# Optimization experiments

Measured on AMD Instinct MI355X. Metric: run time of the kernel, lower is better.

Reference implementation:

```python
import jax, jax.numpy as jnp
import numpy as np

NEG_SLOPE = 0.01  # torch nn.LeakyReLU default


def setup_inputs() -> dict:
    key = jax.random.key(0)
    k1, k2, k3, k4 = jax.random.split(key, 4)
    N, D_IN, D_OUT = 8192, 200, 128
    H = jax.random.normal(k1, (N, D_IN), dtype=jnp.float32)
    A = jax.random.normal(k2, (N, N), dtype=jnp.float32)
    W = jax.random.normal(k3, (D_IN, D_OUT), dtype=jnp.float32) * (1.0 / np.sqrt(D_IN))
    b = jax.random.normal(k4, (D_OUT,), dtype=jnp.float32) * 0.01
    return {"H": H, "A": A, "W": W, "b": b}


def reference(H, A, W, b):
    # A = clamp(sigmoid(A), min=0.1)
    A = jnp.maximum(jax.nn.sigmoid(A), 0.1)
    # D^-1/2 A D^-1/2 -- diag matmuls are equivalent to row/col broadcast scaling
    d_inv_sqrt = jnp.power(A.sum(axis=1), -0.5)  # [N]
    A_hat = A * d_inv_sqrt[:, None] * d_inv_sqrt[None, :]
    # Linear then aggregate
    HW = H @ W + b  # [N, D_OUT]
    out = A_hat @ HW
    out = jnp.where(out >= 0, out, NEG_SLOPE * out)  # LeakyReLU
    return out, A
```

## Files before the change

### kernel.cpp

```cpp
#include <hip/hip_runtime.h>
#include <hip/hip_bf16.h>

#define NR 8192
#define DIN 200
#define DOUT 128

typedef __attribute__((ext_vector_type(8))) short short8;
typedef __attribute__((ext_vector_type(4))) float f32x4;

__device__ __forceinline__ unsigned short f2bf(float x) {
    union { float f; unsigned u; } v; v.f = x;
    unsigned r = v.u + 0x7FFFu + ((v.u >> 16) & 1u);
    return (unsigned short)(r >> 16);
}

__global__ __launch_bounds__(256) void k_sig(const float* __restrict__ A,
                                             float* __restrict__ A2,
                                             float* __restrict__ dis) {
    const int row = blockIdx.x;
    const float4* __restrict__ ar = (const float4*)(A + (size_t)row * NR);
    float4* __restrict__ orow = (float4*)(A2 + (size_t)row * NR);
    float sum = 0.f;
#pragma unroll
    for (int i = 0; i < 8; ++i) {
        const int idx = i * 256 + threadIdx.x;
        float4 x = ar[idx];
        float4 s;
        s.x = fmaxf(__builtin_amdgcn_rcpf(1.f + __expf(-x.x)), 0.1f);
        s.y = fmaxf(__builtin_amdgcn_rcpf(1.f + __expf(-x.y)), 0.1f);
        s.z = fmaxf(__builtin_amdgcn_rcpf(1.f + __expf(-x.z)), 0.1f);
        s.w = fmaxf(__builtin_amdgcn_rcpf(1.f + __expf(-x.w)), 0.1f);
        orow[idx] = s;
        sum += (s.x + s.y) + (s.z + s.w);
    }
#pragma unroll
    for (int off = 32; off > 0; off >>= 1) sum += __shfl_down(sum, off, 64);
    __shared__ float red[4];
    if ((threadIdx.x & 63) == 0) red[threadIdx.x >> 6] = sum;
    __syncthreads();
    if (threadIdx.x == 0)
        dis[row] = __builtin_amdgcn_rsqf((red[0] + red[1]) + (red[2] + red[3]));
}

__global__ __launch_bounds__(256) void k_vt(const float* __restrict__ H,
                                            const float* __restrict__ W,
                                            const float* __restrict__ bias,
                                            const float* __restrict__ dis,
                                            unsigned short* __restrict__ VT) {
    __shared__ float hs[32 * 201];
    const int rowBase = blockIdx.x * 32;
    for (int i = threadIdx.x; i < 32 * DIN; i += 256) {
        int r = i / DIN;
        int k = i - r * DIN;
        hs[r * 201 + k] = H[(size_t)rowBase * DIN + i];
    }
    __syncthreads();
    const int c0 = (threadIdx.x & 31) * 4;
    const int rg = threadIdx.x >> 5;
    float acc[4][4];
#pragma unroll
    for (int r = 0; r < 4; ++r)
#pragma unroll
        for (int i = 0; i < 4; ++i) acc[r][i] = 0.f;
#pragma unroll 4
    for (int k = 0; k < DIN; ++k) {
        float4 w4 = *(const float4*)(W + k * DOUT + c0);
#pragma unroll
        for (int r = 0; r < 4; ++r) {
            float h = hs[(rg * 4 + r) * 201 + k];
            acc[r][0] = fmaf(h, w4.x, acc[r][0]);
            acc[r][1] = fmaf(h, w4.y, acc[r][1]);
            acc[r][2] = fmaf(h, w4.z, acc[r][2]);
            acc[r][3] = fmaf(h, w4.w, acc[r][3]);
        }
    }
    float4 b4 = *(const float4*)(bias + c0);
    float bb[4] = {b4.x, b4.y, b4.z, b4.w};
    float dsc[4];
#pragma unroll
    for (int r = 0; r < 4; ++r) dsc[r] = dis[rowBase + rg * 4 + r];
#pragma unroll
    for (int i = 0; i < 4; ++i) {
        ushort4 pk;
        pk.x = f2bf(dsc[0] * (acc[0][i] + bb[i]));
        pk.y = f2bf(dsc[1] * (acc[1][i] + bb[i]));
        pk.z = f2bf(dsc[2] * (acc[2][i] + bb[i]));
        pk.w = f2bf(dsc[3] * (acc[3][i] + bb[i]));
        *(ushort4*)(VT + (size_t)(c0 + i) * NR + rowBase + rg * 4) = pk;
    }
}

#define BK 32
#define LDK 40
#define NIT 128

__global__ __launch_bounds__(256) void k_gemm(const float* __restrict__ A2,
                                              const unsigned short* __restrict__ VT,
                                              float* __restrict__ P) {
    __shared__ alignas(16) unsigned short lA[2][32 * LDK];
    __shared__ alignas(16) unsigned short lV[2][128 * LDK];
    const int tid = threadIdx.x;
    const int blockRow = blockIdx.x & 255;
    const int s = blockIdx.x >> 8;
    const int rowBase = blockRow * 32;
    const size_t kb0 = (size_t)s * 4096;

    const int am = tid >> 3, ak = (tid & 7) * 4;
    const float* __restrict__ ap = A2 + (size_t)(rowBase + am) * NR + kb0 + ak;
    const int vc = tid >> 2, vq = (tid & 3) * 8;
    const unsigned short* __restrict__ vp0 = VT + (size_t)vc * NR + kb0 + vq;
    const unsigned short* __restrict__ vp1 = vp0 + (size_t)64 * NR;

    const int lane = tid & 63, w = tid >> 6;
    const int rt = w & 1, cg = w >> 1;
    const int fm = lane & 15, kq = lane >> 4;

    f32x4 acc[4];
#pragma unroll
    for (int nt = 0; nt < 4; ++nt) {
        acc[nt][0] = 0.f; acc[nt][1] = 0.f; acc[nt][2] = 0.f; acc[nt][3] = 0.f;
    }

    float4 ga, gv0, gv1;

    ga  = *(const float4*)(ap);
    gv0 = *(const float4*)(vp0);
    gv1 = *(const float4*)(vp1);
    {
        ushort4 pa; pa.x = f2bf(ga.x); pa.y = f2bf(ga.y); pa.z = f2bf(ga.z); pa.w = f2bf(ga.w);
        *(ushort4*)(&lA[0][am * LDK + ak]) = pa;
        *(float4*)(&lV[0][vc * LDK + vq]) = gv0;
        *(float4*)(&lV[0][(vc + 64) * LDK + vq]) = gv1;
    }
    ga  = *(const float4*)(ap + BK);
    gv0 = *(const float4*)(vp0 + BK);
    gv1 = *(const float4*)(vp1 + BK);

    const unsigned short* lap = &lA[0][(rt * 16 + fm) * LDK + kq * 8];
    const unsigned short* lvp = &lV[0][(cg * 64 + fm) * LDK + kq * 8];
    const int strideA = 32 * LDK;
    const int strideV = 128 * LDK;

    for (int i = 0; i < NIT; ++i) {
        __syncthreads();
        if (i + 1 < NIT) {
            const int nb = (i + 1) & 1;
            ushort4 pa; pa.x = f2bf(ga.x); pa.y = f2bf(ga.y); pa.z = f2bf(ga.z); pa.w = f2bf(ga.w);
            *(ushort4*)(&lA[nb][am * LDK + ak]) = pa;
            *(float4*)(&lV[nb][vc * LDK + vq]) = gv0;
            *(float4*)(&lV[nb][(vc + 64) * LDK + vq]) = gv1;
        }
        if (i + 2 < NIT) {
            const size_t off = (size_t)(i + 2) * BK;
            ga  = *(const float4*)(ap + off);
            gv0 = *(const float4*)(vp0 + off);
            gv1 = *(const float4*)(vp1 + off);
        }
        const int cb = i & 1;
        short8 a8 = *(const short8*)(lap + cb * strideA);
#pragma unroll
        for (int nt = 0; nt < 4; ++nt) {
            short8 b8 = *(const short8*)(lvp + cb * strideV + nt * 16 * LDK);
            acc[nt] = __builtin_amdgcn_mfma_f32_16x16x32_bf16(a8, b8, acc[nt], 0, 0, 0);
        }
    }

    float* __restrict__ Pp = P + (size_t)s * ((size_t)NR * DOUT);
    const int row0 = rowBase + rt * 16 + kq * 4;
    const int col0 = cg * 64 + fm;
#pragma unroll
    for (int nt = 0; nt < 4; ++nt) {
#pragma unroll
        for (int v = 0; v < 4; ++v) {
            Pp[(size_t)(row0 + v) * DOUT + col0 + nt * 16] = acc[nt][v];
        }
    }
}

__global__ __launch_bounds__(256) void k_comb(const float* __restrict__ P,
                                              const float* __restrict__ dis,
                                              float* __restrict__ out) {
    const int idx = blockIdx.x * 256 + threadIdx.x;
    const float d = dis[idx >> 5];
    const float4 p0 = *(const float4*)(P + (size_t)idx * 4);
    const float4 p1 = *(const float4*)(P + (size_t)idx * 4 + (size_t)NR * DOUT);
    float4 o;
    o.x = d * (p0.x + p1.x); o.x = o.x >= 0.f ? o.x : 0.01f * o.x;
    o.y = d * (p0.y + p1.y); o.y = o.y >= 0.f ? o.y : 0.01f * o.y;
    o.z = d * (p0.z + p1.z); o.z = o.z >= 0.f ? o.z : 0.01f * o.z;
    o.w = d * (p0.w + p1.w); o.w = o.w >= 0.f ? o.w : 0.01f * o.w;
    *(float4*)(out + (size_t)idx * 4) = o;
}

extern "C" void kernel_launch(void* const* d_in, const int* in_sizes, int n_in,
                              void* d_out, int out_size, void* d_ws, size_t ws_size,
                              hipStream_t stream) {
    const float* H = (const float*)d_in[0];
    const float* A = (const float*)d_in[1];
    const float* W = (const float*)d_in[2];
    const float* b = (const float*)d_in[3];

    float* out = (float*)d_out;
    float* A2  = out + (size_t)NR * DOUT;

    char* ws = (char*)d_ws;
    float* dis = (float*)ws;
    unsigned short* VT = (unsigned short*)(ws + 65536);
    float* P = (float*)(ws + (4u << 20));

    k_sig <<<NR,   256, 0, stream>>>(A, A2, dis);
    k_vt  <<<256,  256, 0, stream>>>(H, W, b, dis, VT);
    k_gemm<<<512,  256, 0, stream>>>(A2, VT, P);
    k_comb<<<1024, 256, 0, stream>>>(P, dis, out);
}
```

Baseline: 585.0 us.

## Emit bf16 copy of sigmoid matrix, drop LDS staging in GEMM, raise K-split

The sigmoid kernel now also writes a bf16 copy of the clamped adjacency, so the aggregation GEMM reads half the bytes and skips the per-iteration fp32-to-bf16 conversion. The GEMM drops LDS double buffering and loads MFMA fragments straight from global memory with register prefetch two steps ahead. The K dimension is split four ways instead of two to launch more blocks, and the combine kernel sums four partials. The projection kernel uses 16 rows per block for more blocks. The costs are an extra 128 MB write in k_sig, uncoalesced short8 fragment loads with no LDS reuse, and more partial-sum traffic.

```diff
diff --git a/kernel.cpp b/kernel.cpp
--- a/kernel.cpp
+++ b/kernel.cpp
@@ -4,6 +4,7 @@
 #define NR 8192
 #define DIN 200
 #define DOUT 128
+#define KSPLIT 4
 
 typedef __attribute__((ext_vector_type(8))) short short8;
 typedef __attribute__((ext_vector_type(4))) float f32x4;
@@ -16,10 +17,12 @@
 
 __global__ __launch_bounds__(256) void k_sig(const float* __restrict__ A,
                                              float* __restrict__ A2,
+                                             unsigned short* __restrict__ A2b,
                                              float* __restrict__ dis) {
     const int row = blockIdx.x;
     const float4* __restrict__ ar = (const float4*)(A + (size_t)row * NR);
     float4* __restrict__ orow = (float4*)(A2 + (size_t)row * NR);
+    ushort4* __restrict__ obr = (ushort4*)(A2b + (size_t)row * NR);
     float sum = 0.f;
 #pragma unroll
     for (int i = 0; i < 8; ++i) {
@@ -31,6 +34,9 @@
         s.z = fmaxf(__builtin_amdgcn_rcpf(1.f + __expf(-x.z)), 0.1f);
         s.w = fmaxf(__builtin_amdgcn_rcpf(1.f + __expf(-x.w)), 0.1f);
         orow[idx] = s;
+        ushort4 pk;
+        pk.x = f2bf(s.x); pk.y = f2bf(s.y); pk.z = f2bf(s.z); pk.w = f2bf(s.w);
+        obr[idx] = pk;
         sum += (s.x + s.y) + (s.z + s.w);
     }
 #pragma unroll
@@ -42,14 +48,15 @@
         dis[row] = __builtin_amdgcn_rsqf((red[0] + red[1]) + (red[2] + red[3]));
 }
 
+#define VROWS 16
 __global__ __launch_bounds__(256) void k_vt(const float* __restrict__ H,
                                             const float* __restrict__ W,
                                             const float* __restrict__ bias,
                                             const float* __restrict__ dis,
                                             unsigned short* __restrict__ VT) {
-    __shared__ float hs[32 * 201];
-    const int rowBase = blockIdx.x * 32;
-    for (int i = threadIdx.x; i < 32 * DIN; i += 256) {
+    __shared__ float hs[VROWS * 201];
+    const int rowBase = blockIdx.x * VROWS;
+    for (int i = threadIdx.x; i < VROWS * DIN; i += 256) {
         int r = i / DIN;
         int k = i - r * DIN;
         hs[r * 201 + k] = H[(size_t)rowBase * DIN + i];
@@ -57,17 +64,17 @@
     __syncthreads();
     const int c0 = (threadIdx.x & 31) * 4;
     const int rg = threadIdx.x >> 5;
-    float acc[4][4];
-#pragma unroll
-    for (int r = 0; r < 4; ++r)
+    float acc[2][4];
+#pragma unroll
+    for (int r = 0; r < 2; ++r)
 #pragma unroll
         for (int i = 0; i < 4; ++i) acc[r][i] = 0.f;
 #pragma unroll 4
     for (int k = 0; k < DIN; ++k) {
         float4 w4 = *(const float4*)(W + k * DOUT + c0);
 #pragma unroll
-        for (int r = 0; r < 4; ++r) {
-            float h = hs[(rg * 4 + r) * 201 + k];
+        for (int r = 0; r < 2; ++r) {
+            float h = hs[(rg * 2 + r) * 201 + k];
             acc[r][0] = fmaf(h, w4.x, acc[r][0]);
             acc[r][1] = fmaf(h, w4.y, acc[r][1]);
             acc[r][2] = fmaf(h, w4.z, acc[r][2]);
@@ -76,93 +83,87 @@
     }
     float4 b4 = *(const float4*)(bias + c0);
     float bb[4] = {b4.x, b4.y, b4.z, b4.w};
-    float dsc[4];
-#pragma unroll
-    for (int r = 0; r < 4; ++r) dsc[r] = dis[rowBase + rg * 4 + r];
+    float d0 = dis[rowBase + rg * 2];
+    float d1 = dis[rowBase + rg * 2 + 1];
 #pragma unroll
     for (int i = 0; i < 4; ++i) {
-        ushort4 pk;
-        pk.x = f2bf(dsc[0] * (acc[0][i] + bb[i]));
-        pk.y = f2bf(dsc[1] * (acc[1][i] + bb[i]));
-        pk.z = f2bf(dsc[2] * (acc[2][i] + bb[i]));
-        pk.w = f2bf(dsc[3] * (acc[3][i] + bb[i]));
-        *(ushort4*)(VT + (size_t)(c0 + i) * NR + rowBase + rg * 4) = pk;
-    }
-}
-
-#define BK 32
-#define LDK 40
-#define NIT 128
-
-__global__ __launch_bounds__(256) void k_gemm(const float* __restrict__ A2,
+        ushort2 pk;
+        pk.x = f2bf(d0 * (acc[0][i] + bb[i]));
+        pk.y = f2bf(d1 * (acc[1][i] + bb[i]));
+        *(ushort2*)(VT + (size_t)(c0 + i) * NR + rowBase + rg * 2) = pk;
+    }
+}
+
+#define KR (NR / KSPLIT)
+#define NI (KR / 32)
+
+__global__ __launch_bounds__(256) void k_gemm(const unsigned short* __restrict__ A2b,
                                               const unsigned short* __restrict__ VT,
                                               float* __restrict__ P) {
-    __shared__ alignas(16) unsigned short lA[2][32 * LDK];
-    __shared__ alignas(16) unsigned short lV[2][128 * LDK];
     const int tid = threadIdx.x;
     const int blockRow = blockIdx.x & 255;
     const int s = blockIdx.x >> 8;
     const int rowBase = blockRow * 32;
-    const size_t kb0 = (size_t)s * 4096;
-
-    const int am = tid >> 3, ak = (tid & 7) * 4;
-    const float* __restrict__ ap = A2 + (size_t)(rowBase + am) * NR + kb0 + ak;
-    const int vc = tid >> 2, vq = (tid & 3) * 8;
-    const unsigned short* __restrict__ vp0 = VT + (size_t)vc * NR + kb0 + vq;
-    const unsigned short* __restrict__ vp1 = vp0 + (size_t)64 * NR;
+    const int kb0 = s * KR;
 
     const int lane = tid & 63, w = tid >> 6;
     const int rt = w & 1, cg = w >> 1;
     const int fm = lane & 15, kq = lane >> 4;
 
+    const unsigned short* __restrict__ ap =
+        A2b + (size_t)(rowBase + rt * 16 + fm) * NR + kb0 + kq * 8;
+    const unsigned short* __restrict__ bp =
+        VT + (size_t)(cg * 64 + fm) * NR + kb0 + kq * 8;
+    const size_t cstep = (size_t)16 * NR;
+
     f32x4 acc[4];
 #pragma unroll
     for (int nt = 0; nt < 4; ++nt) {
         acc[nt][0] = 0.f; acc[nt][1] = 0.f; acc[nt][2] = 0.f; acc[nt][3] = 0.f;
     }
 
-    float4 ga, gv0, gv1;
-
-    ga  = *(const float4*)(ap);
-    gv0 = *(const float4*)(vp0);
-    gv1 = *(const float4*)(vp1);
-    {
-        ushort4 pa; pa.x = f2bf(ga.x); pa.y = f2bf(ga.y); pa.z = f2bf(ga.z); pa.w = f2bf(ga.w);
-        *(ushort4*)(&lA[0][am * LDK + ak]) = pa;
-        *(float4*)(&lV[0][vc * LDK + vq]) = gv0;
-        *(float4*)(&lV[0][(vc + 64) * LDK + vq]) = gv1;
-    }
-    ga  = *(const float4*)(ap + BK);
-    gv0 = *(const float4*)(vp0 + BK);
-    gv1 = *(const float4*)(vp1 + BK);
-
-    const unsigned short* lap = &lA[0][(rt * 16 + fm) * LDK + kq * 8];
-    const unsigned short* lvp = &lV[0][(cg * 64 + fm) * LDK + kq * 8];
-    const int strideA = 32 * LDK;
-    const int strideV = 128 * LDK;
-
-    for (int i = 0; i < NIT; ++i) {
-        __syncthreads();
-        if (i + 1 < NIT) {
-            const int nb = (i + 1) & 1;
-            ushort4 pa; pa.x = f2bf(ga.x); pa.y = f2bf(ga.y); pa.z = f2bf(ga.z); pa.w = f2bf(ga.w);
-            *(ushort4*)(&lA[nb][am * LDK + ak]) = pa;
-            *(float4*)(&lV[nb][vc * LDK + vq]) = gv0;
-            *(float4*)(&lV[nb][(vc + 64) * LDK + vq]) = gv1;
-        }
-        if (i + 2 < NIT) {
-            const size_t off = (size_t)(i + 2) * BK;
-            ga  = *(const float4*)(ap + off);
-            gv0 = *(const float4*)(vp0 + off);
-            gv1 = *(const float4*)(vp1 + off);
-        }
-        const int cb = i & 1;
-        short8 a8 = *(const short8*)(lap + cb * strideA);
-#pragma unroll
-        for (int nt = 0; nt < 4; ++nt) {
-            short8 b8 = *(const short8*)(lvp + cb * strideV + nt * 16 * LDK);
-            acc[nt] = __builtin_amdgcn_mfma_f32_16x16x32_bf16(a8, b8, acc[nt], 0, 0, 0);
-        }
+    short8 a0, a1, b0[4], b1[4];
+    a0 = *(const short8*)(ap);
+    b0[0] = *(const short8*)(bp);
+    b0[1] = *(const short8*)(bp + cstep);
+    b0[2] = *(const short8*)(bp + 2 * cstep);
+    b0[3] = *(const short8*)(bp + 3 * cstep);
+    a1 = *(const short8*)(ap + 32);
+    b1[0] = *(const short8*)(bp + 32);
+    b1[1] = *(const short8*)(bp + 32 + cstep);
+    b1[2] = *(const short8*)(bp + 32 + 2 * cstep);
+    b1[3] = *(const short8*)(bp + 32 + 3 * cstep);
+
+    for (int i = 0; i < NI; i += 2) {
+        short8 at = a0, bt0 = b0[0], bt1 = b0[1], bt2 = b0[2], bt3 = b0[3];
+        if (i + 2 < NI) {
+            const unsigned short* a2p = ap + (i + 2) * 32;
+            const unsigned short* b2p = bp + (i + 2) * 32;
+            a0 = *(const short8*)(a2p);
+            b0[0] = *(const short8*)(b2p);
+            b0[1] = *(const short8*)(b2p + cstep);
+            b0[2] = *(const short8*)(b2p + 2 * cstep);
+            b0[3] = *(const short8*)(b2p + 3 * cstep);
+        }
+        acc[0] = __builtin_amdgcn_mfma_f32_16x16x32_bf16(at, bt0, acc[0], 0, 0, 0);
+        acc[1] = __builtin_amdgcn_mfma_f32_16x16x32_bf16(at, bt1, acc[1], 0, 0, 0);
+        acc[2] = __builtin_amdgcn_mfma_f32_16x16x32_bf16(at, bt2, acc[2], 0, 0, 0);
+        acc[3] = __builtin_amdgcn_mfma_f32_16x16x32_bf16(at, bt3, acc[3], 0, 0, 0);
+
+        short8 au = a1, bu0 = b1[0], bu1 = b1[1], bu2 = b1[2], bu3 = b1[3];
+        if (i + 3 < NI) {
+            const unsigned short* a3p = ap + (i + 3) * 32;
+            const unsigned short* b3p = bp + (i + 3) * 32;
+            a1 = *(const short8*)(a3p);
+            b1[0] = *(const short8*)(b3p);
+            b1[1] = *(const short8*)(b3p + cstep);
+            b1[2] = *(const short8*)(b3p + 2 * cstep);
+            b1[3] = *(const short8*)(b3p + 3 * cstep);
+        }
+        acc[0] = __builtin_amdgcn_mfma_f32_16x16x32_bf16(au, bu0, acc[0], 0, 0, 0);
+        acc[1] = __builtin_amdgcn_mfma_f32_16x16x32_bf16(au, bu1, acc[1], 0, 0, 0);
+        acc[2] = __builtin_amdgcn_mfma_f32_16x16x32_bf16(au, bu2, acc[2], 0, 0, 0);
+        acc[3] = __builtin_amdgcn_mfma_f32_16x16x32_bf16(au, bu3, acc[3], 0, 0, 0);
     }
 
     float* __restrict__ Pp = P + (size_t)s * ((size_t)NR * DOUT);
@@ -182,13 +183,17 @@
                                               float* __restrict__ out) {
     const int idx = blockIdx.x * 256 + threadIdx.x;
     const float d = dis[idx >> 5];
-    const float4 p0 = *(const float4*)(P + (size_t)idx * 4);
-    const float4 p1 = *(const float4*)(P + (size_t)idx * 4 + (size_t)NR * DOUT);
+    const size_t st = (size_t)NR * DOUT;
+    const float* base = P + (size_t)idx * 4;
+    float4 p0 = *(const float4*)(base);
+    float4 p1 = *(const float4*)(base + st);
+    float4 p2 = *(const float4*)(base + 2 * st);
+    float4 p3 = *(const float4*)(base + 3 * st);
     float4 o;
-    o.x = d * (p0.x + p1.x); o.x = o.x >= 0.f ? o.x : 0.01f * o.x;
-    o.y = d * (p0.y + p1.y); o.y = o.y >= 0.f ? o.y : 0.01f * o.y;
-    o.z = d * (p0.z + p1.z); o.z = o.z >= 0.f ? o.z : 0.01f * o.z;
-    o.w = d * (p0.w + p1.w); o.w = o.w >= 0.f ? o.w : 0.01f * o.w;
+    o.x = d * ((p0.x + p1.x) + (p2.x + p3.x)); o.x = o.x >= 0.f ? o.x : 0.01f * o.x;
+    o.y = d * ((p0.y + p1.y) + (p2.y + p3.y)); o.y = o.y >= 0.f ? o.y : 0.01f * o.y;
+    o.z = d * ((p0.z + p1.z) + (p2.z + p3.z)); o.z = o.z >= 0.f ? o.z : 0.01f * o.z;
+    o.w = d * ((p0.w + p1.w) + (p2.w + p3.w)); o.w = o.w >= 0.f ? o.w : 0.01f * o.w;
     *(float4*)(out + (size_t)idx * 4) = o;
 }
 
@@ -206,10 +211,11 @@
     char* ws = (char*)d_ws;
     float* dis = (float*)ws;
     unsigned short* VT = (unsigned short*)(ws + 65536);
-    float* P = (float*)(ws + (4u << 20));
-
-    k_sig <<<NR,   256, 0, stream>>>(A, A2, dis);
-    k_vt  <<<256,  256, 0, stream>>>(H, W, b, dis, VT);
-    k_gemm<<<512,  256, 0, stream>>>(A2, VT, P);
-    k_comb<<<1024, 256, 0, stream>>>(P, dis, out);
-}
+    float* P = (float*)(ws + (4ull << 20));
+    unsigned short* A2b = (unsigned short*)(ws + (32ull << 20));
+
+    k_sig <<<NR,          256, 0, stream>>>(A, A2, A2b, dis);
+    k_vt  <<<NR / VROWS,  256, 0, stream>>>(H, W, b, dis, VT);
+    k_gemm<<<256 * KSPLIT,256, 0, stream>>>(A2b, VT, P);
+    k_comb<<<1024,        256, 0, stream>>>(P, dis, out);
+}
```

New measurement: 641.4 us. +9.6%, slower.
